# Performance work log

Measured on AMD Instinct MI355X. Metric: run time of the kernel, lower is better.

Reference implementation:

```python
import jax, jax.numpy as jnp
import numpy as np

L, D, H, d = 16, 1024, 16, 64
NB, BS = 1024, 16        # num physical blocks, block size (tokens per block)
START_POS = 16368        # T = START_POS + L = 16384
SCALE = 1.0 / np.sqrt(d)


def setup_inputs() -> dict:
    key = jax.random.key(0)
    ks = jax.random.split(key, 5)
    return {
        "x": jax.random.normal(ks[0], (L, D), jnp.float32),
        "k_pool": jax.random.normal(ks[1], (NB, BS, H, d), jnp.float32),
        "v_pool": jax.random.normal(ks[2], (NB, BS, H, d), jnp.float32),
        "W_attn": jax.random.normal(ks[3], (D, 3 * D), jnp.float32) * 0.02,
        "b_attn": jnp.zeros((3 * D,), jnp.float32),
        "W_proj": jax.random.normal(ks[4], (D, D), jnp.float32) * 0.02,
        "b_proj": jnp.zeros((D,), jnp.float32),
        "block_ids": jnp.arange(NB, dtype=jnp.int64),
        "start_pos": START_POS,
    }


def reference(x, k_pool, v_pool, W_attn, b_attn, W_proj, b_proj, block_ids, start_pos):
    # QKV projection
    qkv = x @ W_attn + b_attn                      # [L, 3D]
    q, k, v = jnp.split(qkv, 3, axis=-1)
    q = q.reshape(L, H, d)
    k = k.reshape(L, H, d)
    v = v.reshape(L, H, d)

    # paged write of new K/V into the pool
    pos = start_pos + jnp.arange(L)                # logical positions of new tokens
    blk = block_ids[pos // BS]                     # physical block per token
    off = pos % BS
    k_pool = k_pool.at[blk, off].set(k)
    v_pool = v_pool.at[blk, off].set(v)

    # paged read of the full prefix [0, T)
    T = start_pos + L
    k_pos = jnp.arange(T)
    kb = block_ids[k_pos // BS]
    ko = k_pos % BS
    k_cache = k_pool[kb, ko]                       # [T, H, d]
    v_cache = v_pool[kb, ko]                       # [T, H, d]

    # attention: scores [H, L, T]
    scores = jnp.einsum("lhd,thd->hlt", q, k_cache) * SCALE
    mask = k_pos[None, :] > pos[:, None]           # [L, T] future positions
    scores = jnp.where(mask[None, :, :], -jnp.inf, scores)
    attn = jax.nn.softmax(scores.astype(jnp.float32), axis=-1).astype(scores.dtype)

    out = jnp.einsum("hlt,thd->lhd", attn, v_cache).reshape(L, D)
    return out @ W_proj + b_proj
```

## Files before the change

kernel.cpp:

```cpp
#include <hip/hip_runtime.h>
#include <math.h>

#define L_TOK 16
#define DMODEL 1024
#define NHEAD 16
#define DHEAD 64
#define NBLK 1024
#define BSZ 16
#define START_POS_C 16368
#define TTOT 16384
#define SPLITS 128
#define CHUNK 128
#define KSPLIT 16
#define QSCALE (0.125f * 1.4426950408889634f)

#define OFF_QKVP 0
#define OFF_QW   (OFF_QKVP + KSPLIT * L_TOK * 3 * DMODEL)
#define OFF_ACC  (OFF_QW + NHEAD * L_TOK * DHEAD)
#define OFF_M    (OFF_ACC + NHEAD * SPLITS * L_TOK * DHEAD)
#define OFF_SE   (OFF_M + NHEAD * SPLITS * L_TOK)
#define OFF_ATTN (OFF_SE + NHEAD * SPLITS * L_TOK)
#define OFF_PROJP (OFF_ATTN + L_TOK * DMODEL)

typedef _Float16 half4_t __attribute__((ext_vector_type(4)));
typedef _Float16 half8_t __attribute__((ext_vector_type(8)));
typedef float float4v __attribute__((ext_vector_type(4)));

union H8 { _Float16 h[8]; half8_t v; };
union H4 { _Float16 h[4]; half4_t v; };

__global__ __launch_bounds__(256) void gemm_part(const float* __restrict__ x,
                                                 const float* __restrict__ W,
                                                 float* __restrict__ part,
                                                 int ncols) {
    const int lane = threadIdx.x & 63;
    const int wv = threadIdx.x >> 6;
    const int n = blockIdx.x * 256 + lane * 4;
    const int k0 = blockIdx.y * (DMODEL / KSPLIT);
    const float* xr = x + (size_t)(wv * 4) * DMODEL;
    float4v a0 = {0.f,0.f,0.f,0.f}, a1 = a0, a2 = a0, a3 = a0;
#pragma unroll 4
    for (int k = k0; k < k0 + DMODEL / KSPLIT; ++k) {
        float4v w4 = *(const float4v*)&W[(size_t)k * ncols + n];
        float x0 = xr[k];
        float x1 = xr[DMODEL + k];
        float x2 = xr[2 * DMODEL + k];
        float x3 = xr[3 * DMODEL + k];
        a0 += w4 * x0;
        a1 += w4 * x1;
        a2 += w4 * x2;
        a3 += w4 * x3;
    }
    size_t base = ((size_t)blockIdx.y * L_TOK + wv * 4) * ncols + n;
    *(float4v*)&part[base] = a0;
    *(float4v*)&part[base + (size_t)ncols] = a1;
    *(float4v*)&part[base + 2 * (size_t)ncols] = a2;
    *(float4v*)&part[base + 3 * (size_t)ncols] = a3;
}

__global__ __launch_bounds__(256) void qkv_reduce_scatter(const float* __restrict__ part,
                                                          const float* __restrict__ b_attn,
                                                          const int* __restrict__ block_ids,
                                                          float* __restrict__ qws,
                                                          float* __restrict__ kpool,
                                                          float* __restrict__ vpool) {
    int tid = blockIdx.x * 256 + threadIdx.x;
    int n = tid % (3 * DMODEL);
    int l = tid / (3 * DMODEL);
    float s = b_attn[n];
#pragma unroll
    for (int kb = 0; kb < KSPLIT; ++kb)
        s += part[((size_t)kb * L_TOK + l) * (3 * DMODEL) + n];
    int sec = n >> 10;
    int m = n & (DMODEL - 1);
    int h = m >> 6;
    int dd = m & 63;
    if (sec == 0) {
        qws[(h * L_TOK + l) * DHEAD + dd] = s * QSCALE;
    } else {
        int pos = START_POS_C + l;
        int blk = block_ids[pos >> 4];
        int off = pos & 15;
        size_t idx = (((size_t)blk * BSZ + off) * NHEAD + h) * DHEAD + dd;
        if (sec == 1) kpool[idx] = s;
        else          vpool[idx] = s;
    }
}

__global__ __launch_bounds__(256, 4) void paged_attn(const float* __restrict__ kpool,
                                                     const float* __restrict__ vpool,
                                                     const int* __restrict__ block_ids,
                                                     const float* __restrict__ qws,
                                                     float* __restrict__ accws,
                                                     float* __restrict__ m_arr,
                                                     float* __restrict__ se_arr) {
    const int h = blockIdx.x;
    const int s = blockIdx.y;
    const int tid = threadIdx.x;
    const int w = tid >> 6;
    const int lane = tid & 63;
    const int c = lane & 15;
    const int quad = lane >> 4;

    __shared__ __align__(16) float sacc[4][16][68];
    __shared__ float sm[4][16], sse[4][16];

    const int pb0 = block_ids[s * 8 + 2 * w];
    const int pb1 = block_ids[s * 8 + 2 * w + 1];
    const int tb0 = s * CHUNK + w * 32;
    const int tb1 = tb0 + 16;

    const float* qr = qws + ((size_t)(h * L_TOK + c)) * DHEAD + quad * 8;
    float4 q0 = *(const float4*)(qr);
    float4 q1 = *(const float4*)(qr + 4);
    float4 q2 = *(const float4*)(qr + 32);
    float4 q3 = *(const float4*)(qr + 36);
    const float* kr0 = kpool + (((size_t)pb0 * BSZ + c) * NHEAD + h) * DHEAD + quad * 8;
    const float* kr1 = kpool + (((size_t)pb1 * BSZ + c) * NHEAD + h) * DHEAD + quad * 8;
    float4 k0a = *(const float4*)(kr0);      float4 k0b = *(const float4*)(kr0 + 4);
    float4 k0c = *(const float4*)(kr0 + 32); float4 k0d = *(const float4*)(kr0 + 36);
    float4 k1a = *(const float4*)(kr1);      float4 k1b = *(const float4*)(kr1 + 4);
    float4 k1c = *(const float4*)(kr1 + 32); float4 k1d = *(const float4*)(kr1 + 36);
    float v0[4][4], v1[4][4];
    {
        const float* vb0 = vpool + ((size_t)pb0 * BSZ * NHEAD + h) * DHEAD + c;
        const float* vb1 = vpool + ((size_t)pb1 * BSZ * NHEAD + h) * DHEAD + c;
#pragma unroll
        for (int j = 0; j < 4; ++j) {
            const float* r0 = vb0 + (size_t)(4 * quad + j) * (NHEAD * DHEAD);
            const float* r1 = vb1 + (size_t)(4 * quad + j) * (NHEAD * DHEAD);
#pragma unroll
            for (int ndv = 0; ndv < 4; ++ndv) {
                v0[j][ndv] = r0[16 * ndv];
                v1[j][ndv] = r1[16 * ndv];
            }
        }
    }

    H8 qb0, qb1;
    qb0.h[0]=(_Float16)q0.x; qb0.h[1]=(_Float16)q0.y; qb0.h[2]=(_Float16)q0.z; qb0.h[3]=(_Float16)q0.w;
    qb0.h[4]=(_Float16)q1.x; qb0.h[5]=(_Float16)q1.y; qb0.h[6]=(_Float16)q1.z; qb0.h[7]=(_Float16)q1.w;
    qb1.h[0]=(_Float16)q2.x; qb1.h[1]=(_Float16)q2.y; qb1.h[2]=(_Float16)q2.z; qb1.h[3]=(_Float16)q2.w;
    qb1.h[4]=(_Float16)q3.x; qb1.h[5]=(_Float16)q3.y; qb1.h[6]=(_Float16)q3.z; qb1.h[7]=(_Float16)q3.w;

    const float4v z4 = {0.f, 0.f, 0.f, 0.f};
    H8 ka, kb;
    ka.h[0]=(_Float16)k0a.x; ka.h[1]=(_Float16)k0a.y; ka.h[2]=(_Float16)k0a.z; ka.h[3]=(_Float16)k0a.w;
    ka.h[4]=(_Float16)k0b.x; ka.h[5]=(_Float16)k0b.y; ka.h[6]=(_Float16)k0b.z; ka.h[7]=(_Float16)k0b.w;
    kb.h[0]=(_Float16)k0c.x; kb.h[1]=(_Float16)k0c.y; kb.h[2]=(_Float16)k0c.z; kb.h[3]=(_Float16)k0c.w;
    kb.h[4]=(_Float16)k0d.x; kb.h[5]=(_Float16)k0d.y; kb.h[6]=(_Float16)k0d.z; kb.h[7]=(_Float16)k0d.w;
    float4v st0 = __builtin_amdgcn_mfma_f32_16x16x32_f16(ka.v, qb0.v, z4, 0, 0, 0);
    st0 = __builtin_amdgcn_mfma_f32_16x16x32_f16(kb.v, qb1.v, st0, 0, 0, 0);
    ka.h[0]=(_Float16)k1a.x; ka.h[1]=(_Float16)k1a.y; ka.h[2]=(_Float16)k1a.z; ka.h[3]=(_Float16)k1a.w;
    ka.h[4]=(_Float16)k1b.x; ka.h[5]=(_Float16)k1b.y; ka.h[6]=(_Float16)k1b.z; ka.h[7]=(_Float16)k1b.w;
    kb.h[0]=(_Float16)k1c.x; kb.h[1]=(_Float16)k1c.y; kb.h[2]=(_Float16)k1c.z; kb.h[3]=(_Float16)k1c.w;
    kb.h[4]=(_Float16)k1d.x; kb.h[5]=(_Float16)k1d.y; kb.h[6]=(_Float16)k1d.z; kb.h[7]=(_Float16)k1d.w;
    float4v st1 = __builtin_amdgcn_mfma_f32_16x16x32_f16(ka.v, qb0.v, z4, 0, 0, 0);
    st1 = __builtin_amdgcn_mfma_f32_16x16x32_f16(kb.v, qb1.v, st1, 0, 0, 0);

    if (tb0 + 15 > START_POS_C) {
#pragma unroll
        for (int r = 0; r < 4; ++r)
            if (tb0 + 4 * quad + r > START_POS_C + c) st0[r] = -INFINITY;
    }
    if (tb1 + 15 > START_POS_C) {
#pragma unroll
        for (int r = 0; r < 4; ++r)
            if (tb1 + 4 * quad + r > START_POS_C + c) st1[r] = -INFINITY;
    }

    float tm = fmaxf(fmaxf(fmaxf(st0[0], st0[1]), fmaxf(st0[2], st0[3])),
                     fmaxf(fmaxf(st1[0], st1[1]), fmaxf(st1[2], st1[3])));
    tm = fmaxf(tm, __shfl_xor(tm, 16, 64));
    tm = fmaxf(tm, __shfl_xor(tm, 32, 64));
    H4 pa0, pa1;
    pa0.h[0]=(_Float16)exp2f(st0[0]-tm); pa0.h[1]=(_Float16)exp2f(st0[1]-tm);
    pa0.h[2]=(_Float16)exp2f(st0[2]-tm); pa0.h[3]=(_Float16)exp2f(st0[3]-tm);
    pa1.h[0]=(_Float16)exp2f(st1[0]-tm); pa1.h[1]=(_Float16)exp2f(st1[1]-tm);
    pa1.h[2]=(_Float16)exp2f(st1[2]-tm); pa1.h[3]=(_Float16)exp2f(st1[3]-tm);
    float ts = ((float)pa0.h[0] + (float)pa0.h[1]) + ((float)pa0.h[2] + (float)pa0.h[3])
             + ((float)pa1.h[0] + (float)pa1.h[1]) + ((float)pa1.h[2] + (float)pa1.h[3]);
    ts += __shfl_xor(ts, 16, 64);
    ts += __shfl_xor(ts, 32, 64);

    float4v acc[4];
#pragma unroll
    for (int i = 0; i < 4; ++i) acc[i] = z4;
#pragma unroll
    for (int ndv = 0; ndv < 4; ++ndv) {
        H4 bf;
        bf.h[0]=(_Float16)v0[0][ndv]; bf.h[1]=(_Float16)v0[1][ndv];
        bf.h[2]=(_Float16)v0[2][ndv]; bf.h[3]=(_Float16)v0[3][ndv];
        acc[ndv] = __builtin_amdgcn_mfma_f32_16x16x16f16(pa0.v, bf.v, acc[ndv], 0, 0, 0);
        bf.h[0]=(_Float16)v1[0][ndv]; bf.h[1]=(_Float16)v1[1][ndv];
        bf.h[2]=(_Float16)v1[2][ndv]; bf.h[3]=(_Float16)v1[3][ndv];
        acc[ndv] = __builtin_amdgcn_mfma_f32_16x16x16f16(pa1.v, bf.v, acc[ndv], 0, 0, 0);
    }

#pragma unroll
    for (int ndv = 0; ndv < 4; ++ndv)
#pragma unroll
        for (int r = 0; r < 4; ++r)
            sacc[w][4 * quad + r][16 * ndv + c] = acc[ndv][r];
    if (quad == 0) { sm[w][c] = tm; sse[w][c] = ts; }
    __syncthreads();

    const int q = tid >> 4;
    const int dseg = tid & 15;
    float m0 = sm[0][q], m1 = sm[1][q], m2 = sm[2][q], m3 = sm[3][q];
    float M = fmaxf(fmaxf(m0, m1), fmaxf(m2, m3));
    float u0 = exp2f(m0 - M), u1 = exp2f(m1 - M), u2 = exp2f(m2 - M), u3 = exp2f(m3 - M);
    float den = u0 * sse[0][q] + u1 * sse[1][q] + u2 * sse[2][q] + u3 * sse[3][q];
    float4v num = u0 * (*(const float4v*)&sacc[0][q][4 * dseg])
                + u1 * (*(const float4v*)&sacc[1][q][4 * dseg])
                + u2 * (*(const float4v*)&sacc[2][q][4 * dseg])
                + u3 * (*(const float4v*)&sacc[3][q][4 * dseg]);
    const size_t ob = ((size_t)(h * SPLITS + s) * L_TOK + q) * DHEAD + 4 * dseg;
    *(float4v*)&accws[ob] = num;
    if (dseg == 0) {
        const size_t mb = (size_t)(h * SPLITS + s) * L_TOK + q;
        m_arr[mb] = M;
        se_arr[mb] = den;
    }
}

__global__ __launch_bounds__(256) void combine(const float* __restrict__ accws,
                                               const float* __restrict__ m_arr,
                                               const float* __restrict__ se_arr,
                                               float* __restrict__ attnws) {
    const int h = blockIdx.x >> 4;
    const int l = blockIdx.x & 15;
    const int w = threadIdx.x >> 6;
    const int lane = threadIdx.x & 63;
    __shared__ float sm[4], sse[4], sacc[4][64];

    float M = -INFINITY, num = 0.f, den = 0.f;
#pragma unroll 4
    for (int s = w; s < SPLITS; s += 4) {
        const size_t idx = (size_t)(h * SPLITS + s) * L_TOK + l;
        const float ms = m_arr[idx];
        const float ses = se_arr[idx];
        const float a = accws[idx * DHEAD + lane];
        const float Mn = fmaxf(M, ms);
        const float c_old = exp2f(M - Mn);
        const float c_new = exp2f(ms - Mn);
        num = num * c_old + a * c_new;
        den = den * c_old + ses * c_new;
        M = Mn;
    }
    if (lane == 0) { sm[w] = M; sse[w] = den; }
    sacc[w][lane] = num;
    __syncthreads();
    if (w == 0) {
        const float M0 = fmaxf(fmaxf(sm[0], sm[1]), fmaxf(sm[2], sm[3]));
        float nn = 0.f, dd = 0.f;
#pragma unroll
        for (int i = 0; i < 4; ++i) {
            const float wgt = exp2f(sm[i] - M0);
            nn = fmaf(wgt, sacc[i][lane], nn);
            dd = fmaf(wgt, sse[i], dd);
        }
        attnws[(size_t)l * DMODEL + h * DHEAD + lane] = nn / dd;
    }
}

__global__ __launch_bounds__(256) void proj_reduce(const float* __restrict__ part,
                                                   const float* __restrict__ bias,
                                                   float* __restrict__ out) {
    int tid = blockIdx.x * 256 + threadIdx.x;
    int n = tid & (DMODEL - 1);
    int l = tid >> 10;
    float s = bias[n];
#pragma unroll
    for (int kb = 0; kb < KSPLIT; ++kb)
        s += part[((size_t)kb * L_TOK + l) * DMODEL + n];
    out[tid] = s;
}

extern "C" void kernel_launch(void* const* d_in, const int* in_sizes, int n_in,
                              void* d_out, int out_size, void* d_ws, size_t ws_size,
                              hipStream_t stream) {
    const float* x       = (const float*)d_in[0];
    float* kpool         = (float*)d_in[1];
    float* vpool         = (float*)d_in[2];
    const float* W_attn  = (const float*)d_in[3];
    const float* b_attn  = (const float*)d_in[4];
    const float* W_proj  = (const float*)d_in[5];
    const float* b_proj  = (const float*)d_in[6];
    const int* block_ids = (const int*)d_in[7];
    float* ws  = (float*)d_ws;
    float* out = (float*)d_out;

    gemm_part<<<dim3(12, KSPLIT), 256, 0, stream>>>(x, W_attn, ws + OFF_QKVP, 3 * DMODEL);
    qkv_reduce_scatter<<<192, 256, 0, stream>>>(ws + OFF_QKVP, b_attn, block_ids,
                                                ws + OFF_QW, kpool, vpool);
    paged_attn<<<dim3(NHEAD, SPLITS), 256, 0, stream>>>(kpool, vpool, block_ids,
                                                        ws + OFF_QW, ws + OFF_ACC,
                                                        ws + OFF_M, ws + OFF_SE);
    combine<<<NHEAD * L_TOK, 256, 0, stream>>>(ws + OFF_ACC, ws + OFF_M, ws + OFF_SE,
                                               ws + OFF_ATTN);
    gemm_part<<<dim3(4, KSPLIT), 256, 0, stream>>>(ws + OFF_ATTN, W_proj, ws + OFF_PROJP, DMODEL);
    proj_reduce<<<64, 256, 0, stream>>>(ws + OFF_PROJP, b_proj, out);
}
```

Before: 208.1 us.

## Restructure GEMM tiling, two-pass combine, and add sched barrier in attention

The split-K GEMM kernel now stages a transposed 64x16 slice of x in shared memory, and each thread computes all 16 tokens for two columns. This cuts redundant x loads and halves the grid. The combine kernel replaces the online rescaling loop with a max pass followed by a weighted-sum pass, which removes per-step exp2 rescales and the serial dependency. A sched_barrier after the K/V loads in paged_attn stops the compiler from interleaving the conversions with the loads. The GEMM grid is smaller (96 and 32 blocks), which may underfill the GPU.

```diff
diff --git a/kernel.cpp b/kernel.cpp
--- a/kernel.cpp
+++ b/kernel.cpp
@@ -25,37 +25,51 @@
 typedef _Float16 half4_t __attribute__((ext_vector_type(4)));
 typedef _Float16 half8_t __attribute__((ext_vector_type(8)));
 typedef float float4v __attribute__((ext_vector_type(4)));
+typedef float float2v __attribute__((ext_vector_type(2)));
 
 union H8 { _Float16 h[8]; half8_t v; };
 union H4 { _Float16 h[4]; half4_t v; };
 
-__global__ __launch_bounds__(256) void gemm_part(const float* __restrict__ x,
-                                                 const float* __restrict__ W,
-                                                 float* __restrict__ part,
-                                                 int ncols) {
+__global__ __launch_bounds__(256) void gemm16(const float* __restrict__ x,
+                                              const float* __restrict__ W,
+                                              float* __restrict__ part,
+                                              int ncols) {
     const int lane = threadIdx.x & 63;
     const int wv = threadIdx.x >> 6;
-    const int n = blockIdx.x * 256 + lane * 4;
+    const int col = blockIdx.x * 512 + wv * 128 + lane * 2;
     const int k0 = blockIdx.y * (DMODEL / KSPLIT);
-    const float* xr = x + (size_t)(wv * 4) * DMODEL;
-    float4v a0 = {0.f,0.f,0.f,0.f}, a1 = a0, a2 = a0, a3 = a0;
-#pragma unroll 4
-    for (int k = k0; k < k0 + DMODEL / KSPLIT; ++k) {
-        float4v w4 = *(const float4v*)&W[(size_t)k * ncols + n];
-        float x0 = xr[k];
-        float x1 = xr[DMODEL + k];
-        float x2 = xr[2 * DMODEL + k];
-        float x3 = xr[3 * DMODEL + k];
-        a0 += w4 * x0;
-        a1 += w4 * x1;
-        a2 += w4 * x2;
-        a3 += w4 * x3;
-    }
-    size_t base = ((size_t)blockIdx.y * L_TOK + wv * 4) * ncols + n;
-    *(float4v*)&part[base] = a0;
-    *(float4v*)&part[base + (size_t)ncols] = a1;
-    *(float4v*)&part[base + 2 * (size_t)ncols] = a2;
-    *(float4v*)&part[base + 3 * (size_t)ncols] = a3;
+
+    __shared__ __align__(16) float sxT[64 * 16];
+#pragma unroll
+    for (int i = threadIdx.x; i < 64 * 16; i += 256) {
+        int k = i & 63, l = i >> 6;
+        sxT[k * 16 + l] = x[(size_t)l * DMODEL + k0 + k];
+    }
+    __syncthreads();
+
+    float2v acc[16];
+#pragma unroll
+    for (int l = 0; l < 16; ++l) acc[l] = (float2v){0.f, 0.f};
+
+#pragma unroll 8
+    for (int k = 0; k < 64; ++k) {
+        float2v w2 = *(const float2v*)&W[(size_t)(k0 + k) * ncols + col];
+        const float4v* xk = (const float4v*)&sxT[k * 16];
+        float4v xa = xk[0], xb = xk[1], xc = xk[2], xd = xk[3];
+        acc[0]  += w2 * xa[0];  acc[1]  += w2 * xa[1];
+        acc[2]  += w2 * xa[2];  acc[3]  += w2 * xa[3];
+        acc[4]  += w2 * xb[0];  acc[5]  += w2 * xb[1];
+        acc[6]  += w2 * xb[2];  acc[7]  += w2 * xb[3];
+        acc[8]  += w2 * xc[0];  acc[9]  += w2 * xc[1];
+        acc[10] += w2 * xc[2];  acc[11] += w2 * xc[3];
+        acc[12] += w2 * xd[0];  acc[13] += w2 * xd[1];
+        acc[14] += w2 * xd[2];  acc[15] += w2 * xd[3];
+    }
+
+    const size_t base = ((size_t)blockIdx.y * L_TOK) * ncols + col;
+#pragma unroll
+    for (int l = 0; l < 16; ++l)
+        *(float2v*)&part[base + (size_t)l * ncols] = acc[l];
 }
 
 __global__ __launch_bounds__(256) void qkv_reduce_scatter(const float* __restrict__ part,
@@ -136,6 +150,7 @@
             }
         }
     }
+    __builtin_amdgcn_sched_barrier(0);
 
     H8 qb0, qb1;
     qb0.h[0]=(_Float16)q0.x; qb0.h[1]=(_Float16)q0.y; qb0.h[2]=(_Float16)q0.z; qb0.h[3]=(_Float16)q0.w;
@@ -234,20 +249,25 @@
     const int lane = threadIdx.x & 63;
     __shared__ float sm[4], sse[4], sacc[4][64];
 
-    float M = -INFINITY, num = 0.f, den = 0.f;
-#pragma unroll 4
-    for (int s = w; s < SPLITS; s += 4) {
-        const size_t idx = (size_t)(h * SPLITS + s) * L_TOK + l;
-        const float ms = m_arr[idx];
-        const float ses = se_arr[idx];
-        const float a = accws[idx * DHEAD + lane];
-        const float Mn = fmaxf(M, ms);
-        const float c_old = exp2f(M - Mn);
-        const float c_new = exp2f(ms - Mn);
-        num = num * c_old + a * c_new;
-        den = den * c_old + ses * c_new;
-        M = Mn;
-    }
+    const size_t base = (size_t)h * SPLITS * L_TOK + l;
+
+    float mreg[SPLITS / 4];
+#pragma unroll
+    for (int i = 0; i < SPLITS / 4; ++i)
+        mreg[i] = m_arr[base + (size_t)(w + 4 * i) * L_TOK];
+    float M = -INFINITY;
+#pragma unroll
+    for (int i = 0; i < SPLITS / 4; ++i) M = fmaxf(M, mreg[i]);
+
+    float num = 0.f, den = 0.f;
+#pragma unroll
+    for (int i = 0; i < SPLITS / 4; ++i) {
+        const size_t idx = base + (size_t)(w + 4 * i) * L_TOK;
+        const float wgt = exp2f(mreg[i] - M);
+        num = fmaf(wgt, accws[idx * DHEAD + lane], num);
+        den = fmaf(wgt, se_arr[idx], den);
+    }
+
     if (lane == 0) { sm[w] = M; sse[w] = den; }
     sacc[w][lane] = num;
     __syncthreads();
@@ -291,7 +311,7 @@
     float* ws  = (float*)d_ws;
     float* out = (float*)d_out;
 
-    gemm_part<<<dim3(12, KSPLIT), 256, 0, stream>>>(x, W_attn, ws + OFF_QKVP, 3 * DMODEL);
+    gemm16<<<dim3(6, KSPLIT), 256, 0, stream>>>(x, W_attn, ws + OFF_QKVP, 3 * DMODEL);
     qkv_reduce_scatter<<<192, 256, 0, stream>>>(ws + OFF_QKVP, b_attn, block_ids,
                                                 ws + OFF_QW, kpool, vpool);
     paged_attn<<<dim3(NHEAD, SPLITS), 256, 0, stream>>>(kpool, vpool, block_ids,
@@ -299,6 +319,6 @@
                                                         ws + OFF_M, ws + OFF_SE);
     combine<<<NHEAD * L_TOK, 256, 0, stream>>>(ws + OFF_ACC, ws + OFF_M, ws + OFF_SE,
                                                ws + OFF_ATTN);
-    gemm_part<<<dim3(4, KSPLIT), 256, 0, stream>>>(ws + OFF_ATTN, W_proj, ws + OFF_PROJP, DMODEL);
+    gemm16<<<dim3(2, KSPLIT), 256, 0, stream>>>(ws + OFF_ATTN, W_proj, ws + OFF_PROJP, DMODEL);
     proj_reduce<<<64, 256, 0, stream>>>(ws + OFF_PROJP, b_proj, out);
 }
```

Result: slower. 247.5 us (+18.9%).
